# Optimization experiments

Hardware: AMD Instinct MI355X
Metric: run time of the kernel (lower is better)

Reference implementation:

```python
import jax, jax.numpy as jnp
import numpy as np

ATOM_DIM = 64
BOND_DIM = 64
B, N_ATOMS, N_BONDS = 32, 256, 512


def setup_inputs() -> dict:
    key = jax.random.key(0)
    k1, k2, k3, k4 = jax.random.split(key, 4)
    atom_state = jax.random.normal(k1, (B, N_ATOMS, ATOM_DIM), dtype=jnp.float32)
    bond_state = jax.random.normal(k2, (B, N_BONDS, BOND_DIM), dtype=jnp.float32)
    connectivity = jax.random.randint(k3, (B, N_BONDS, 2), 0, N_ATOMS, dtype=jnp.int64)
    # glorot-ish scale for the learned bond->matrix projection
    scale = (2.0 / (BOND_DIM + ATOM_DIM * ATOM_DIM)) ** 0.5
    bond_transform = jax.random.normal(k4, (BOND_DIM, ATOM_DIM * ATOM_DIM), dtype=jnp.float32) * scale
    return {
        "atom_state": atom_state,
        "bond_state": bond_state,
        "connectivity": connectivity,
        "bond_transform": bond_transform,
    }


def reference(atom_state, bond_state, connectivity, bond_transform):
    # src atom per edge: gather along atom axis with batch dim (tf.gather batch_dims=1)
    src_idx = connectivity[:, :, 0]                                  # [B, E]
    src_atoms = jnp.take_along_axis(
        atom_state, src_idx[:, :, None], axis=1)                    # [B, E, D]
    # bond embedding -> per-edge DxD matrix
    W = bond_transform.reshape(BOND_DIM, ATOM_DIM, ATOM_DIM)         # [K, D, D]
    bond_weights = jnp.einsum('bek,kij->beij', bond_state, W)        # [B, E, D, D]
    # per-edge matrix-vector message: A_e @ h_src
    messages = jnp.einsum('beij,bej->bei', bond_weights, src_atoms)  # [B, E, D]
    return messages
```

## Files before the change

kernel.cpp:

```cpp
#include <hip/hip_runtime.h>
#include <stdint.h>


#define NATOMS 256
#define DIM 64
#define BM 64

typedef _Float16 f16;
typedef _Float16 f16x2 __attribute__((ext_vector_type(2)));
typedef _Float16 f16x8 __attribute__((ext_vector_type(8)));
typedef float f32x16 __attribute__((ext_vector_type(16)));

union H8 { f16x8 v8; f16x2 v2[4]; };

__global__ __launch_bounds__(256) void prep_w2f(const float* __restrict__ bt,
                                                f16* __restrict__ w2f) {
    const int d  = blockIdx.x * 256 + threadIdx.x;
    const int kg = d >> 9, c = d & 511;
    const int wcq = c >> 8, s = (c >> 6) & 3, l = c & 63;
    const int i = (l & 31) + 32 * wcq;
    const int u = 2 * s + (l >> 5);
    const float* src = bt + (size_t)kg * 4096 + i * 64 + u * 8;
    const float4 p = *reinterpret_cast<const float4*>(src);
    const float4 q = *reinterpret_cast<const float4*>(src + 4);
    const f16x8 h = { (f16)p.x, (f16)p.y, (f16)p.z, (f16)p.w,
                      (f16)q.x, (f16)q.y, (f16)q.z, (f16)q.w };
    reinterpret_cast<f16x8*>(w2f)[d] = h;
}

static __device__ __forceinline__ unsigned swz16(unsigned lane) {
    return (lane * 16u) ^ ((lane & 0x38u) << 1);
}

__global__ __launch_bounds__(512, 2) void bond_msg(
    const float* __restrict__ atom, const float* __restrict__ bond,
    const int* __restrict__ conn, const f16* __restrict__ w2f,
    float* __restrict__ out)
{
    __shared__ __align__(16) unsigned char smem[65536];

    const int tid  = threadIdx.x;
    const int lane = tid & 63;
    const int w    = tid >> 6;
    const int wc   = w & 1;
    const int kq   = w >> 1;
    const int lo   = lane & 31;
    const int hi   = lane >> 5;
    const int blk  = blockIdx.x;
    const int bond0 = blk * BM;

    const int m0 = lo, m1 = lo + 32;
    const int ia0 = conn[(bond0 + m0) * 2];
    const int ia1 = conn[(bond0 + m1) * 2];

    f16x2 bp0[16], bp1[16];
    {
        const float* br0 = bond + (size_t)(bond0 + m0) * DIM + kq * 16;
        const float* br1 = bond + (size_t)(bond0 + m1) * DIM + kq * 16;
        #pragma unroll
        for (int q = 0; q < 4; ++q) {
            const float4 v0 = *reinterpret_cast<const float4*>(br0 + q * 4);
            const float4 v1 = *reinterpret_cast<const float4*>(br1 + q * 4);
            const f16 a0 = (f16)v0.x, a1 = (f16)v0.y, a2 = (f16)v0.z, a3 = (f16)v0.w;
            const f16 c0 = (f16)v1.x, c1 = (f16)v1.y, c2 = (f16)v1.z, c3 = (f16)v1.w;
            bp0[q*4+0] = (f16x2){a0,a0}; bp0[q*4+1] = (f16x2){a1,a1};
            bp0[q*4+2] = (f16x2){a2,a2}; bp0[q*4+3] = (f16x2){a3,a3};
            bp1[q*4+0] = (f16x2){c0,c0}; bp1[q*4+1] = (f16x2){c1,c1};
            bp1[q*4+2] = (f16x2){c2,c2}; bp1[q*4+3] = (f16x2){c3,c3};
        }
    }

    const float* ar0 = atom + (size_t)(blk >> 3) * (NATOMS * DIM) + (size_t)ia0 * DIM;
    const float* ar1 = atom + (size_t)(blk >> 3) * (NATOMS * DIM) + (size_t)ia1 * DIM;
    f16x2 srcv[2][4][4];
    #pragma unroll
    for (int s = 0; s < 4; ++s) {
        const int j0 = s * 16 + hi * 8;
        float4 p0 = *reinterpret_cast<const float4*>(ar0 + j0);
        float4 p1 = *reinterpret_cast<const float4*>(ar0 + j0 + 4);
        float4 q0 = *reinterpret_cast<const float4*>(ar1 + j0);
        float4 q1 = *reinterpret_cast<const float4*>(ar1 + j0 + 4);
        srcv[0][s][0] = (f16x2){ (f16)p0.x, (f16)p0.y };
        srcv[0][s][1] = (f16x2){ (f16)p0.z, (f16)p0.w };
        srcv[0][s][2] = (f16x2){ (f16)p1.x, (f16)p1.y };
        srcv[0][s][3] = (f16x2){ (f16)p1.z, (f16)p1.w };
        srcv[1][s][0] = (f16x2){ (f16)q0.x, (f16)q0.y };
        srcv[1][s][1] = (f16x2){ (f16)q0.z, (f16)q0.w };
        srcv[1][s][2] = (f16x2){ (f16)q1.x, (f16)q1.y };
        srcv[1][s][3] = (f16x2){ (f16)q1.z, (f16)q1.w };
    }

    const char* gw = reinterpret_cast<const char*>(w2f)
                   + (size_t)kq * 16 * 8192 + wc * 4096 + lane * 16;

    f16x8 b0[4], b1[4], b2[4], b3[4];
    f32x16 acc0 = {}, acc1 = {};

    #define LOADIT(buf, itw) do { if ((itw) < 16) {                       \
        const char* _p = gw + (itw) * 8192;                               \
        buf[0] = *reinterpret_cast<const f16x8*>(_p);                     \
        buf[1] = *reinterpret_cast<const f16x8*>(_p + 1024);              \
        buf[2] = *reinterpret_cast<const f16x8*>(_p + 2048);              \
        buf[3] = *reinterpret_cast<const f16x8*>(_p + 3072);              \
    } } while (0)

    #define COMPIT(buf, iti) do {                                         \
        const f16x2 _c0 = bp0[iti];                                       \
        const f16x2 _c1 = bp1[iti];                                       \
        _Pragma("unroll")                                                 \
        for (int s = 0; s < 4; ++s) {                                     \
            H8 _a0, _a1;                                                  \
            _Pragma("unroll")                                             \
            for (int t = 0; t < 4; ++t) {                                 \
                _a0.v2[t] = _c0 * srcv[0][s][t];                          \
                _a1.v2[t] = _c1 * srcv[1][s][t];                          \
            }                                                             \
            acc0 = __builtin_amdgcn_mfma_f32_32x32x16_f16(_a0.v8, buf[s], acc0, 0, 0, 0); \
            acc1 = __builtin_amdgcn_mfma_f32_32x32x16_f16(_a1.v8, buf[s], acc1, 0, 0, 0); \
        }                                                                 \
    } while (0)

    LOADIT(b0, 0); LOADIT(b1, 1); LOADIT(b2, 2);

    #pragma unroll
    for (int it = 0; it < 16; it += 4) {
        LOADIT(b3, it + 3);
        COMPIT(b0, it + 0);
        LOADIT(b0, it + 4);
        COMPIT(b1, it + 1);
        LOADIT(b1, it + 5);
        COMPIT(b2, it + 2);
        LOADIT(b2, it + 6);
        COMPIT(b3, it + 3);
    }

    {
        const unsigned wbase = (unsigned)w * 8192u;
        const unsigned so = swz16((unsigned)lane);
        #pragma unroll
        for (int g = 0; g < 4; ++g) {
            float4 v0 = { acc0[4*g+0], acc0[4*g+1], acc0[4*g+2], acc0[4*g+3] };
            *reinterpret_cast<float4*>(smem + wbase + g*1024 + so) = v0;
            float4 v1 = { acc1[4*g+0], acc1[4*g+1], acc1[4*g+2], acc1[4*g+3] };
            *reinterpret_cast<float4*>(smem + wbase + (g+4)*1024 + so) = v1;
        }
    }
    __syncthreads();
    {
        const int c  = tid & 63;
        const int rb = tid >> 6;
        const int a  = rb >> 2, g = rb & 3;
        const unsigned colb = (unsigned)(c & 31);
        const unsigned wcs  = (unsigned)(c >> 5);
        const unsigned o0 = swz16(colb);
        const unsigned o1 = swz16(32u + colb);
        float4 s0 = {0.f,0.f,0.f,0.f}, s1 = {0.f,0.f,0.f,0.f};
        #pragma unroll
        for (int q = 0; q < 4; ++q) {
            const unsigned base = (unsigned)((q*2 + wcs) * 8192 + (a*4+g) * 1024);
            const float4 u0 = *reinterpret_cast<const float4*>(smem + base + o0);
            const float4 u1 = *reinterpret_cast<const float4*>(smem + base + o1);
            s0.x += u0.x; s0.y += u0.y; s0.z += u0.z; s0.w += u0.w;
            s1.x += u1.x; s1.y += u1.y; s1.z += u1.z; s1.w += u1.w;
        }
        float* orow = out + (size_t)(bond0 + 32*a + 8*g) * 64 + c;
        orow[0*64] = s0.x; orow[1*64] = s0.y; orow[2*64] = s0.z; orow[3*64] = s0.w;
        orow[4*64] = s1.x; orow[5*64] = s1.y; orow[6*64] = s1.z; orow[7*64] = s1.w;
    }
    #undef LOADIT
    #undef COMPIT
}

__global__ __launch_bounds__(256) void bond_fallback(
    const float* __restrict__ atom, const float* __restrict__ bond,
    const int* __restrict__ conn, const float* __restrict__ bt,
    float* __restrict__ out)
{
    __shared__ float Wk[4096];
    __shared__ float srcs[4][64];
    __shared__ float bnds[4][64];
    const int blk = blockIdx.x;
    const int e0 = blk * 4;
    const int b = e0 >> 9;
    const int t = threadIdx.x;
    const int il = t & 63, eg = t >> 6;
    const int e = e0 + eg;
    const int ia = conn[e * 2];
    srcs[eg][il] = atom[(size_t)b * (NATOMS * DIM) + (size_t)ia * DIM + il];
    bnds[eg][il] = bond[(size_t)e * DIM + il];
    float acc = 0.f;
    for (int k = 0; k < 64; ++k) {
        __syncthreads();
        #pragma unroll
        for (int c = 0; c < 4; ++c) {
            float4 v = reinterpret_cast<const float4*>(bt + (size_t)k * 4096)[t + c * 256];
            reinterpret_cast<float4*>(Wk)[t + c * 256] = v;
        }
        __syncthreads();
        float s = 0.f;
        #pragma unroll
        for (int j = 0; j < 64; ++j) s += Wk[il * 64 + j] * srcs[eg][j];
        acc += bnds[eg][k] * s;
    }
    out[(size_t)e * DIM + il] = acc;
}

extern "C" void kernel_launch(void* const* d_in, const int* in_sizes, int n_in,
                              void* d_out, int out_size, void* d_ws, size_t ws_size,
                              hipStream_t stream) {
    const float* atom = (const float*)d_in[0];
    const float* bond = (const float*)d_in[1];
    const int*   conn = (const int*)d_in[2];
    const float* bt   = (const float*)d_in[3];
    float* out = (float*)d_out;

    if (ws_size >= (size_t)64 * 4096 * sizeof(f16)) {
        f16* w2f = (f16*)d_ws;
        prep_w2f<<<128, 256, 0, stream>>>(bt, w2f);
        bond_msg<<<256, 512, 0, stream>>>(atom, bond, conn, w2f, out);
    } else {
        bond_fallback<<<4096, 256, 0, stream>>>(atom, bond, conn, bt, out);
    }
}
```

Baseline: 22.92 us.

## Stream weight fragments into LDS with async global_load_lds ring buffer

The per-wave register prefetch of the f16 weight fragments is replaced by direct global-to-LDS asynchronous copies (global_load_lds, 16 bytes per lane) into a 4-slot ring per wave. Explicit vmcnt waits and sched barriers pace the 16 k-iterations, and MFMA B-operands are read back from LDS. This frees the registers that held four in-flight weight buffers and keeps the loads in flight without the compiler reordering them. In exchange, shared memory grows to 128 KB per block, which limits residency to one block per CU, and the hand-counted vmcnt values depend on the exact order in which loads are issued.

```diff
diff --git a/kernel.cpp b/kernel.cpp
--- a/kernel.cpp
+++ b/kernel.cpp
@@ -11,7 +11,14 @@
 typedef _Float16 f16x8 __attribute__((ext_vector_type(8)));
 typedef float f32x16 __attribute__((ext_vector_type(16)));
 
+#define AS1 __attribute__((address_space(1)))
+#define AS3 __attribute__((address_space(3)))
+
 union H8 { f16x8 v8; f16x2 v2[4]; };
+
+static __device__ __forceinline__ void gll16(const void* g, void* l) {
+    __builtin_amdgcn_global_load_lds((AS1 void*)(uintptr_t)g, (AS3 void*)l, 16, 0, 0);
+}
 
 __global__ __launch_bounds__(256) void prep_w2f(const float* __restrict__ bt,
                                                 f16* __restrict__ w2f) {
@@ -37,7 +44,7 @@
     const int* __restrict__ conn, const f16* __restrict__ w2f,
     float* __restrict__ out)
 {
-    __shared__ __align__(16) unsigned char smem[65536];
+    __shared__ __align__(16) unsigned char smem[131072];
 
     const int tid  = threadIdx.x;
     const int lane = tid & 63;
@@ -52,6 +59,22 @@
     const int m0 = lo, m1 = lo + 32;
     const int ia0 = conn[(bond0 + m0) * 2];
     const int ia1 = conn[(bond0 + m1) * 2];
+
+    const char* gw = reinterpret_cast<const char*>(w2f)
+                   + (size_t)(kq * 16) * 8192 + wc * 4096 + lane * 16;
+    char* lsta = reinterpret_cast<char*>(smem) + w * 16384;
+    const char* lread = reinterpret_cast<const char*>(smem) + w * 16384 + lane * 16;
+
+    #define ISSUE(itf) do {                                               \
+        const char* _g = gw + (itf) * 8192;                               \
+        char* _l = lsta + ((itf) & 3) * 4096;                             \
+        gll16(_g,        _l);                                             \
+        gll16(_g + 1024, _l + 1024);                                      \
+        gll16(_g + 2048, _l + 2048);                                      \
+        gll16(_g + 3072, _l + 3072);                                      \
+    } while (0)
+
+    ISSUE(0); ISSUE(1); ISSUE(2);
 
     f16x2 bp0[16], bp1[16];
     {
@@ -90,50 +113,43 @@
         srcv[1][s][3] = (f16x2){ (f16)q1.z, (f16)q1.w };
     }
 
-    const char* gw = reinterpret_cast<const char*>(w2f)
-                   + (size_t)kq * 16 * 8192 + wc * 4096 + lane * 16;
-
-    f16x8 b0[4], b1[4], b2[4], b3[4];
     f32x16 acc0 = {}, acc1 = {};
 
-    #define LOADIT(buf, itw) do { if ((itw) < 16) {                       \
-        const char* _p = gw + (itw) * 8192;                               \
-        buf[0] = *reinterpret_cast<const f16x8*>(_p);                     \
-        buf[1] = *reinterpret_cast<const f16x8*>(_p + 1024);              \
-        buf[2] = *reinterpret_cast<const f16x8*>(_p + 2048);              \
-        buf[3] = *reinterpret_cast<const f16x8*>(_p + 3072);              \
-    } } while (0)
-
-    #define COMPIT(buf, iti) do {                                         \
+    #define COMPIT(iti) do {                                              \
+        const char* _lr = lread + ((iti) & 3) * 4096;                     \
         const f16x2 _c0 = bp0[iti];                                       \
         const f16x2 _c1 = bp1[iti];                                       \
         _Pragma("unroll")                                                 \
         for (int s = 0; s < 4; ++s) {                                     \
+            const f16x8 bf = *reinterpret_cast<const f16x8*>(_lr + s * 1024); \
             H8 _a0, _a1;                                                  \
             _Pragma("unroll")                                             \
             for (int t = 0; t < 4; ++t) {                                 \
                 _a0.v2[t] = _c0 * srcv[0][s][t];                          \
                 _a1.v2[t] = _c1 * srcv[1][s][t];                          \
             }                                                             \
-            acc0 = __builtin_amdgcn_mfma_f32_32x32x16_f16(_a0.v8, buf[s], acc0, 0, 0, 0); \
-            acc1 = __builtin_amdgcn_mfma_f32_32x32x16_f16(_a1.v8, buf[s], acc1, 0, 0, 0); \
+            acc0 = __builtin_amdgcn_mfma_f32_32x32x16_f16(_a0.v8, bf, acc0, 0, 0, 0); \
+            acc1 = __builtin_amdgcn_mfma_f32_32x32x16_f16(_a1.v8, bf, acc1, 0, 0, 0); \
         }                                                                 \
     } while (0)
 
-    LOADIT(b0, 0); LOADIT(b1, 1); LOADIT(b2, 2);
-
-    #pragma unroll
-    for (int it = 0; it < 16; it += 4) {
-        LOADIT(b3, it + 3);
-        COMPIT(b0, it + 0);
-        LOADIT(b0, it + 4);
-        COMPIT(b1, it + 1);
-        LOADIT(b1, it + 5);
-        COMPIT(b2, it + 2);
-        LOADIT(b2, it + 6);
-        COMPIT(b3, it + 3);
-    }
-
+    #define STEP(iti, wtxt) do {                                          \
+        if ((iti) + 3 < 16) ISSUE((iti) + 3);                             \
+        asm volatile("s_waitcnt vmcnt(" wtxt ")" ::: "memory");           \
+        __builtin_amdgcn_sched_barrier(0);                                \
+        COMPIT(iti);                                                      \
+    } while (0)
+
+    STEP( 0, "12"); STEP( 1, "12"); STEP( 2, "12"); STEP( 3, "12");
+    STEP( 4, "12"); STEP( 5, "12"); STEP( 6, "12"); STEP( 7, "12");
+    STEP( 8, "12"); STEP( 9, "12"); STEP(10, "12"); STEP(11, "12");
+    STEP(12, "12"); STEP(13, "8");  STEP(14, "4");  STEP(15, "0");
+
+    #undef STEP
+    #undef COMPIT
+    #undef ISSUE
+
+    __syncthreads();
     {
         const unsigned wbase = (unsigned)w * 8192u;
         const unsigned so = swz16((unsigned)lane);
@@ -167,8 +183,6 @@
         orow[0*64] = s0.x; orow[1*64] = s0.y; orow[2*64] = s0.z; orow[3*64] = s0.w;
         orow[4*64] = s1.x; orow[5*64] = s1.y; orow[6*64] = s1.z; orow[7*64] = s1.w;
     }
-    #undef LOADIT
-    #undef COMPIT
 }
 
 __global__ __launch_bounds__(256) void bond_fallback(
```

New measurement: 24.25 us. +5.8%, slower.
